# Kernel optimization log

Hardware: AMD Instinct MI355X
Metric: run time of the kernel (lower is better)

Reference implementation:

```python
import jax, jax.numpy as jnp
import numpy as np

B, N, FIN, FOUT, E = 2, 50000, 128, 64, 800000


def setup_inputs() -> dict:
    key = jax.random.key(0)
    ks = jax.random.split(key, 7)
    x = jax.random.normal(ks[0], (B, N, FIN), dtype=jnp.float32)
    W = jax.random.normal(ks[1], (FIN, FOUT), dtype=jnp.float32) * (1.0 / np.sqrt(FIN))
    W_self = jax.random.normal(ks[2], (FIN, FOUT), dtype=jnp.float32) * (1.0 / np.sqrt(FIN))
    b_self = jax.random.normal(ks[3], (FOUT,), dtype=jnp.float32) * 0.01
    edge_row = jax.random.randint(ks[4], (E,), 0, N, dtype=jnp.int32)
    edge_col = jax.random.randint(ks[5], (E,), 0, N, dtype=jnp.int32)
    edge_val = jax.random.uniform(ks[6], (E,), dtype=jnp.float32)
    return {"x": x, "W": W, "W_self": W_self, "b_self": b_self,
            "edge_row": edge_row, "edge_col": edge_col, "edge_val": edge_val}


def reference(x, W, W_self, b_self, edge_row, edge_col, edge_val):
    # x: (B, N, FIN); adjacency in COO form: out[r] += val * in[c]
    Bn, Nn, _ = x.shape
    Fo = W.shape[1]
    x_trans = jnp.einsum("bnf,fo->bno", x, W)               # (B, N, FOUT), no bias
    # Same layout trick as torch: sparse.mm over (N, B*FOUT)
    xr = x_trans.transpose(1, 0, 2).reshape(Nn, Bn * Fo)    # (N, B*FOUT)
    msgs = edge_val[:, None] * xr[edge_col]                  # (E, B*FOUT) gather
    agg = jax.ops.segment_sum(msgs, edge_row, num_segments=Nn)  # (N, B*FOUT) scatter-add
    agg = agg.reshape(Nn, Bn, Fo).transpose(1, 0, 2)         # (B, N, FOUT)
    self_c = jnp.einsum("bnf,fo->bno", x, W_self) + b_self   # Linear with bias
    return jax.nn.relu(self_c + agg)
```

## Files before the change

### kernel.cpp

```cpp
#include <hip/hip_runtime.h>
#include <hip/hip_fp16.h>

#define Bc   2
#define Nn   50000
#define FINc 128
#define FOUTc 64
#define Mtot (Bc * Nn)
#define CCOMB 128
#define GB 1563
#define EB4 782
#define NB 196
#define ZTOT (Nn * 16 + 256)

typedef __bf16 bf16x8 __attribute__((ext_vector_type(8)));
typedef float  f32x4  __attribute__((ext_vector_type(4)));

static __device__ inline unsigned short f2bf(float f) {
    unsigned int u = __float_as_uint(f);
    u += 0x7fffu + ((u >> 16) & 1u);
    return (unsigned short)(u >> 16);
}

__global__ __launch_bounds__(256) void prep(
    const float* __restrict__ W, const float* __restrict__ Ws,
    unsigned short* __restrict__ Bp, int* __restrict__ zbase)
{
    if (blockIdx.x < 8) {
        const int idx = blockIdx.x * 256 + threadIdx.x;
        const int lane = idx & 63;
        const int kt   = (idx >> 6) & 3;
        const int nt   = idx >> 8;
        const int n    = nt * 16 + (lane & 15);
        const int k0   = kt * 32 + (lane >> 4) * 8;
        unsigned short o8[8];
#pragma unroll
        for (int j = 0; j < 8; ++j) {
            const int f = k0 + j;
            const float v = (n < 64) ? W[f * FOUTc + n] : Ws[f * FOUTc + (n - 64)];
            o8[j] = f2bf(v);
        }
        *(uint4*)&Bp[(size_t)idx * 8] = *(uint4*)o8;
    } else {
        const int i4 = (blockIdx.x - 8) * 1024 + threadIdx.x * 4;
        if (i4 + 4 <= ZTOT)
            *(int4*)&zbase[i4] = make_int4(0, 0, 0, 0);
    }
}

__global__ __launch_bounds__(256) void count_edges(
    const int* __restrict__ erow, int* __restrict__ cntp,
    int* __restrict__ rank, int E)
{
    const int base = blockIdx.x * 1024 + threadIdx.x * 4;
    if (base + 4 > E) return;
    const int4 r4 = *(const int4*)&erow[base];
    const int k0 = atomicAdd(&cntp[(size_t)r4.x * 16], 1);
    const int k1 = atomicAdd(&cntp[(size_t)r4.y * 16], 1);
    const int k2 = atomicAdd(&cntp[(size_t)r4.z * 16], 1);
    const int k3 = atomicAdd(&cntp[(size_t)r4.w * 16], 1);
    *(int4*)&rank[base] = make_int4(k0, k1, k2, k3);
}

__global__ __launch_bounds__(256) void gemm_mfma(
    const float* __restrict__ x, const unsigned short* __restrict__ Bp,
    const float* __restrict__ bself,
    unsigned short* __restrict__ xrb, unsigned short* __restrict__ selfb)
{
    const int lane = threadIdx.x & 63;
    const int quad = lane >> 4;
    const int mbase = blockIdx.x * 64 + (threadIdx.x >> 6) * 16;

    const int mrow   = mbase + (lane & 15);
    const int mclamp = (mrow < Mtot) ? mrow : (Mtot - 1);
    const float* __restrict__ xrow = &x[(size_t)mclamp * FINc];

    f32x4 acc[8] = {};

#pragma unroll
    for (int kt = 0; kt < 4; ++kt) {
        const int k0 = kt * 32 + quad * 8;
        const float4 xa = *(const float4*)&xrow[k0];
        const float4 xb = *(const float4*)&xrow[k0 + 4];
        bf16x8 bf;
        bf[0] = (__bf16)xa.x; bf[1] = (__bf16)xa.y;
        bf[2] = (__bf16)xa.z; bf[3] = (__bf16)xa.w;
        bf[4] = (__bf16)xb.x; bf[5] = (__bf16)xb.y;
        bf[6] = (__bf16)xb.z; bf[7] = (__bf16)xb.w;

        const bf16x8* __restrict__ abase =
            (const bf16x8*)&Bp[(size_t)(kt * 64 + lane) * 8];
#pragma unroll
        for (int nt = 0; nt < 8; ++nt) {
            const bf16x8 af = abase[nt * 4 * 64];
            acc[nt] = __builtin_amdgcn_mfma_f32_16x16x32_bf16(af, bf, acc[nt], 0, 0, 0);
        }
    }

    const int m = mbase + (lane & 15);
    if (m < Mtot) {
        const int b = (m >= Nn) ? 1 : 0;
        const int n = m - b * Nn;
        unsigned short* __restrict__ xp = &xrb[(size_t)n * CCOMB + b * FOUTc];
        const int cq = quad * 4;
#pragma unroll
        for (int nt = 0; nt < 4; ++nt) {
            const int c = nt * 16 + cq;
            unsigned short h[4];
            h[0] = f2bf(acc[nt][0]); h[1] = f2bf(acc[nt][1]);
            h[2] = f2bf(acc[nt][2]); h[3] = f2bf(acc[nt][3]);
            *(uint2*)&xp[c] = *(uint2*)h;
        }
        unsigned short* __restrict__ sp = &selfb[(size_t)m * FOUTc];
#pragma unroll
        for (int nt = 4; nt < 8; ++nt) {
            const int o = (nt - 4) * 16 + cq;
            const float4 b4 = *(const float4*)&bself[o];
            unsigned short h[4];
            h[0] = f2bf(acc[nt][0] + b4.x); h[1] = f2bf(acc[nt][1] + b4.y);
            h[2] = f2bf(acc[nt][2] + b4.z); h[3] = f2bf(acc[nt][3] + b4.w);
            *(uint2*)&sp[o] = *(uint2*)h;
        }
    }
}

__global__ __launch_bounds__(256) void scan_fill(
    const int* __restrict__ cntp, int* __restrict__ aggf,
    int* __restrict__ rowstart, int E)
{
    __shared__ int s[256];
    const int t = threadIdx.x, b = blockIdx.x;
    const int idx = b * 256 + t;
    const int v = (idx < Nn) ? cntp[(size_t)idx * 16] : 0;

    s[t] = v;
    __syncthreads();
    for (int off = 1; off < 256; off <<= 1) {
        const int add = (t >= off) ? s[t - off] : 0;
        __syncthreads();
        s[t] += add;
        __syncthreads();
    }
    const int excl  = s[t] - v;
    const int total = s[255];

    if (t == 0) atomicOr(&aggf[b], (total << 1) | 1);

    int a = 0;
    if (t < b) {
        int w;
        do { w = atomicOr(&aggf[t], 0); } while (!(w & 1));
        a = w >> 1;
    }
    __syncthreads();
    s[t] = a;
    __syncthreads();
    for (int off = 128; off > 0; off >>= 1) {
        if (t < off) s[t] += s[t + off];
        __syncthreads();
    }
    const int pre = s[0];

    if (idx < Nn) rowstart[idx] = pre + excl;
    if (b == 0 && t == 0) rowstart[Nn] = E;
}

__global__ __launch_bounds__(256) void bucket(
    const int* __restrict__ erow, const int* __restrict__ ecol,
    const float* __restrict__ evalv, const int* __restrict__ rank,
    const int* __restrict__ rowstart, unsigned int* __restrict__ cvp, int E)
{
    const int base = blockIdx.x * 1024 + threadIdx.x * 4;
    if (base + 4 > E) return;
    const int4   r4 = *(const int4*)&erow[base];
    const int4   c4 = *(const int4*)&ecol[base];
    const float4 v4 = *(const float4*)&evalv[base];
    const int4   k4 = *(const int4*)&rank[base];
    cvp[rowstart[r4.x] + k4.x] =
        ((unsigned int)__half_as_ushort(__float2half(v4.x)) << 17) | (unsigned int)c4.x;
    cvp[rowstart[r4.y] + k4.y] =
        ((unsigned int)__half_as_ushort(__float2half(v4.y)) << 17) | (unsigned int)c4.y;
    cvp[rowstart[r4.z] + k4.z] =
        ((unsigned int)__half_as_ushort(__float2half(v4.z)) << 17) | (unsigned int)c4.z;
    cvp[rowstart[r4.w] + k4.w] =
        ((unsigned int)__half_as_ushort(__float2half(v4.w)) << 17) | (unsigned int)c4.w;
}

#define GATH8(EIDX, ACC)                                                      \
    {                                                                         \
        const unsigned int w = cvp[EIDX];                                     \
        const float vv = __half2float(__ushort_as_half(                       \
                             (unsigned short)(w >> 17)));                     \
        const uint4 raw = *(const uint4*)&xrb[(size_t)(w & 0x1FFFFu) * CCOMB + c0]; \
        ACC[0] = fmaf(vv, __uint_as_float(raw.x << 16),         ACC[0]);      \
        ACC[1] = fmaf(vv, __uint_as_float(raw.x & 0xffff0000u), ACC[1]);      \
        ACC[2] = fmaf(vv, __uint_as_float(raw.y << 16),         ACC[2]);      \
        ACC[3] = fmaf(vv, __uint_as_float(raw.y & 0xffff0000u), ACC[3]);      \
        ACC[4] = fmaf(vv, __uint_as_float(raw.z << 16),         ACC[4]);      \
        ACC[5] = fmaf(vv, __uint_as_float(raw.z & 0xffff0000u), ACC[5]);      \
        ACC[6] = fmaf(vv, __uint_as_float(raw.w << 16),         ACC[6]);      \
        ACC[7] = fmaf(vv, __uint_as_float(raw.w & 0xffff0000u), ACC[7]);      \
    }

__global__ __launch_bounds__(256) void row_gather(
    const int* __restrict__ rowstart, const unsigned int* __restrict__ cvp,
    const unsigned short* __restrict__ xrb, const unsigned short* __restrict__ selfb,
    float* __restrict__ outp)
{
    const int j    = blockIdx.x;
    const int low3 = j & 7;
    const int h    = (low3 >= 4) ? 1 : 0;
    const int ord  = (j >> 3) * 4 + (low3 & 3);
    int n = ord * 4 + (threadIdx.x >> 6);
    n = __builtin_amdgcn_readfirstlane(n);

    const int lane = threadIdx.x & 63;
    const int slot = lane >> 3;
    const int c0   = h * 64 + (lane & 7) * 8;

    const int s    = rowstart[n];
    const int eend = rowstart[n + 1];

    float aA[8] = {0.f, 0.f, 0.f, 0.f, 0.f, 0.f, 0.f, 0.f};
    float aB[8] = {0.f, 0.f, 0.f, 0.f, 0.f, 0.f, 0.f, 0.f};

    int e = s;
    for (; e + 16 <= eend; e += 16) {
        GATH8(e + slot,     aA);
        GATH8(e + 8 + slot, aB);
    }
    if (e + 8 <= eend) {
        GATH8(e + slot, aA);
        e += 8;
    }
    if (e + slot < eend) GATH8(e + slot, aB);

#pragma unroll
    for (int i = 0; i < 8; ++i) {
        aA[i] += aB[i];
        aA[i] += __shfl_down(aA[i], 8);
        aA[i] += __shfl_down(aA[i], 16);
        aA[i] += __shfl_down(aA[i], 32);
    }

    if (lane < 8) {
        const size_t m = (size_t)h * Nn + n;
        const int o = lane * 8;
        const uint4 sb = *(const uint4*)&selfb[m * FOUTc + o];
        float sv[8];
        sv[0] = __uint_as_float(sb.x << 16); sv[1] = __uint_as_float(sb.x & 0xffff0000u);
        sv[2] = __uint_as_float(sb.y << 16); sv[3] = __uint_as_float(sb.y & 0xffff0000u);
        sv[4] = __uint_as_float(sb.z << 16); sv[5] = __uint_as_float(sb.z & 0xffff0000u);
        sv[6] = __uint_as_float(sb.w << 16); sv[7] = __uint_as_float(sb.w & 0xffff0000u);
        float4 s0, s1;
        s0.x = fmaxf(sv[0] + aA[0], 0.0f); s0.y = fmaxf(sv[1] + aA[1], 0.0f);
        s0.z = fmaxf(sv[2] + aA[2], 0.0f); s0.w = fmaxf(sv[3] + aA[3], 0.0f);
        s1.x = fmaxf(sv[4] + aA[4], 0.0f); s1.y = fmaxf(sv[5] + aA[5], 0.0f);
        s1.z = fmaxf(sv[6] + aA[6], 0.0f); s1.w = fmaxf(sv[7] + aA[7], 0.0f);
        float* __restrict__ op = &outp[m * FOUTc + o];
        *(float4*)&op[0] = s0;
        *(float4*)&op[4] = s1;
    }
}

extern "C" void kernel_launch(void* const* d_in, const int* in_sizes, int n_in,
                              void* d_out, int out_size, void* d_ws, size_t ws_size,
                              hipStream_t stream)
{
    const float* x    = (const float*)d_in[0];
    const float* W    = (const float*)d_in[1];
    const float* Ws   = (const float*)d_in[2];
    const float* bs   = (const float*)d_in[3];
    const int*   erow = (const int*)d_in[4];
    const int*   ecol = (const int*)d_in[5];
    const float* eval = (const float*)d_in[6];
    float* outp = (float*)d_out;
    const int E = in_sizes[4];

    unsigned short* xrb   = (unsigned short*)d_ws;
    unsigned short* selfb = xrb + (size_t)Nn * CCOMB;
    unsigned int*   cvp   = (unsigned int*)(selfb + (size_t)Mtot * FOUTc);
    int* rank     = (int*)(cvp + E);
    int* rowstart = rank + E;
    int* cntp     = rowstart + (Nn + 8);
    int* aggf     = cntp + (size_t)Nn * 16;
    unsigned short* Bp = (unsigned short*)(aggf + 256);

    prep<<<8 + (ZTOT + 1023) / 1024, 256, 0, stream>>>(W, Ws, Bp, cntp);

    count_edges<<<EB4, 256, 0, stream>>>(erow, cntp, rank, E);

    gemm_mfma<<<GB, 256, 0, stream>>>(x, Bp, bs, xrb, selfb);

    scan_fill<<<NB, 256, 0, stream>>>(cntp, aggf, rowstart, E);

    bucket<<<EB4, 256, 0, stream>>>(erow, ecol, eval, rank, rowstart, cvp, E);

    row_gather<<<Nn / 2, 256, 0, stream>>>(rowstart, cvp, xrb, selfb, outp);
}
```

Baseline: 213.4 us.

## Fuse edge counting into GEMM launch, preload x rows, simplify gather loop

Merges the count_edges and gemm_mfma kernels into one launch whose first EB4 blocks do the atomic edge counting and whose remaining blocks do the MFMA GEMM. This removes one launch and lets the atomic-bound counting overlap with the bandwidth-bound GEMM. The GEMM also loads all of its x row fragments up front so the memory requests are in flight together. The row gather loop is reduced from two accumulators with unrolled tails to a single strided loop, which may lower memory-level parallelism in exchange for fewer registers and simpler control flow.

After: 213.1 us. No clear change (-0.2%).

```diff
diff --git a/kernel.cpp b/kernel.cpp
--- a/kernel.cpp
+++ b/kernel.cpp
@@ -47,40 +47,47 @@
     }
 }
 
-__global__ __launch_bounds__(256) void count_edges(
+__global__ __launch_bounds__(256) void gemm_count(
+    const float* __restrict__ x, const unsigned short* __restrict__ Bp,
+    const float* __restrict__ bself,
+    unsigned short* __restrict__ xrb, unsigned short* __restrict__ selfb,
     const int* __restrict__ erow, int* __restrict__ cntp,
     int* __restrict__ rank, int E)
 {
-    const int base = blockIdx.x * 1024 + threadIdx.x * 4;
-    if (base + 4 > E) return;
-    const int4 r4 = *(const int4*)&erow[base];
-    const int k0 = atomicAdd(&cntp[(size_t)r4.x * 16], 1);
-    const int k1 = atomicAdd(&cntp[(size_t)r4.y * 16], 1);
-    const int k2 = atomicAdd(&cntp[(size_t)r4.z * 16], 1);
-    const int k3 = atomicAdd(&cntp[(size_t)r4.w * 16], 1);
-    *(int4*)&rank[base] = make_int4(k0, k1, k2, k3);
-}
-
-__global__ __launch_bounds__(256) void gemm_mfma(
-    const float* __restrict__ x, const unsigned short* __restrict__ Bp,
-    const float* __restrict__ bself,
-    unsigned short* __restrict__ xrb, unsigned short* __restrict__ selfb)
-{
+    if (blockIdx.x < EB4) {
+        const int base = blockIdx.x * 1024 + threadIdx.x * 4;
+        if (base + 4 <= E) {
+            const int4 r4 = *(const int4*)&erow[base];
+            const int k0 = atomicAdd(&cntp[(size_t)r4.x * 16], 1);
+            const int k1 = atomicAdd(&cntp[(size_t)r4.y * 16], 1);
+            const int k2 = atomicAdd(&cntp[(size_t)r4.z * 16], 1);
+            const int k3 = atomicAdd(&cntp[(size_t)r4.w * 16], 1);
+            *(int4*)&rank[base] = make_int4(k0, k1, k2, k3);
+        }
+        return;
+    }
+
     const int lane = threadIdx.x & 63;
     const int quad = lane >> 4;
-    const int mbase = blockIdx.x * 64 + (threadIdx.x >> 6) * 16;
+    const int mbase = (blockIdx.x - EB4) * 64 + (threadIdx.x >> 6) * 16;
 
     const int mrow   = mbase + (lane & 15);
     const int mclamp = (mrow < Mtot) ? mrow : (Mtot - 1);
-    const float* __restrict__ xrow = &x[(size_t)mclamp * FINc];
+    const float* __restrict__ xrow = &x[(size_t)mclamp * FINc + quad * 8];
+
+    float4 xv[8];
+#pragma unroll
+    for (int kt = 0; kt < 4; ++kt) {
+        xv[2 * kt]     = *(const float4*)&xrow[kt * 32];
+        xv[2 * kt + 1] = *(const float4*)&xrow[kt * 32 + 4];
+    }
 
     f32x4 acc[8] = {};
 
 #pragma unroll
     for (int kt = 0; kt < 4; ++kt) {
-        const int k0 = kt * 32 + quad * 8;
-        const float4 xa = *(const float4*)&xrow[k0];
-        const float4 xb = *(const float4*)&xrow[k0 + 4];
+        const float4 xa = xv[2 * kt];
+        const float4 xb = xv[2 * kt + 1];
         bf16x8 bf;
         bf[0] = (__bf16)xa.x; bf[1] = (__bf16)xa.y;
         bf[2] = (__bf16)xa.z; bf[3] = (__bf16)xa.w;
@@ -221,22 +228,12 @@
     const int eend = rowstart[n + 1];
 
     float aA[8] = {0.f, 0.f, 0.f, 0.f, 0.f, 0.f, 0.f, 0.f};
-    float aB[8] = {0.f, 0.f, 0.f, 0.f, 0.f, 0.f, 0.f, 0.f};
-
-    int e = s;
-    for (; e + 16 <= eend; e += 16) {
-        GATH8(e + slot,     aA);
-        GATH8(e + 8 + slot, aB);
-    }
-    if (e + 8 <= eend) {
-        GATH8(e + slot, aA);
-        e += 8;
-    }
-    if (e + slot < eend) GATH8(e + slot, aB);
+
+    for (int e = s + slot; e < eend; e += 8)
+        GATH8(e, aA);
 
 #pragma unroll
     for (int i = 0; i < 8; ++i) {
-        aA[i] += aB[i];
         aA[i] += __shfl_down(aA[i], 8);
         aA[i] += __shfl_down(aA[i], 16);
         aA[i] += __shfl_down(aA[i], 32);
@@ -287,9 +284,8 @@
 
     prep<<<8 + (ZTOT + 1023) / 1024, 256, 0, stream>>>(W, Ws, Bp, cntp);
 
-    count_edges<<<EB4, 256, 0, stream>>>(erow, cntp, rank, E);
-
-    gemm_mfma<<<GB, 256, 0, stream>>>(x, Bp, bs, xrb, selfb);
+    gemm_count<<<EB4 + GB, 256, 0, stream>>>(x, Bp, bs, xrb, selfb,
+                                             erow, cntp, rank, E);
 
     scan_fill<<<NB, 256, 0, stream>>>(cntp, aggf, rowstart, E);
 
```
